# Optimization experiments

Hardware: AMD Instinct MI355X
Metric: run time of the kernel (lower is better)

Reference implementation:

```python
import jax, jax.numpy as jnp
from jax import lax
import numpy as np

HIDDEN = 16
INPUT = 1
OUTPUT = 1
BATCH = 8192
SEQ = 512


def setup_inputs() -> dict:
    key = jax.random.key(0)
    ks = jax.random.split(key, 12)
    s = 1.0 / np.sqrt(HIDDEN)  # PyTorch nn.RNN init scale
    u = lambda k, shape: jax.random.uniform(k, shape, jnp.float32, -s, s)
    return {
        "x": jax.random.normal(ks[0], (BATCH, SEQ, INPUT), jnp.float32),
        "W_ih0": u(ks[1], (HIDDEN, INPUT)),
        "W_hh0": u(ks[2], (HIDDEN, HIDDEN)),
        "b_ih0": u(ks[3], (HIDDEN,)),
        "b_hh0": u(ks[4], (HIDDEN,)),
        "W_ih1": u(ks[5], (HIDDEN, HIDDEN)),
        "W_hh1": u(ks[6], (HIDDEN, HIDDEN)),
        "b_ih1": u(ks[7], (HIDDEN,)),
        "b_hh1": u(ks[8], (HIDDEN,)),
        "W_fc": u(ks[9], (OUTPUT, HIDDEN)),
        "b_fc": u(ks[10], (OUTPUT,)),
    }


def reference(x, W_ih0, W_hh0, b_ih0, b_hh0, W_ih1, W_hh1, b_ih1, b_hh1, W_fc, b_fc):
    # x: [B, S, input]; 2-layer tanh RNN (batch_first), zero initial state,
    # then fc applied to the last timestep of the top layer.
    B = x.shape[0]
    h_init = (jnp.zeros((B, HIDDEN), x.dtype), jnp.zeros((B, HIDDEN), x.dtype))

    def step(carry, xt):  # xt: [B, input]
        h0, h1 = carry
        h0 = jnp.tanh(xt @ W_ih0.T + b_ih0 + h0 @ W_hh0.T + b_hh0)
        h1 = jnp.tanh(h0 @ W_ih1.T + b_ih1 + h1 @ W_hh1.T + b_hh1)
        return (h0, h1), None

    xs = jnp.swapaxes(x, 0, 1)  # [S, B, input] for scan over time
    (h0, h1), _ = lax.scan(step, h_init, xs)
    return h1 @ W_fc.T + b_fc  # [B, output]
```

## Files before the change

### kernel.cpp

```cpp
#include <hip/hip_runtime.h>


#define ROTF(v, K) __int_as_float(__builtin_amdgcn_update_dpp( \
    0, __float_as_int(v), 0x120 + (K), 0xF, 0xF, true))

__device__ __forceinline__ float tanh_fast(float v) {
    float e = __builtin_amdgcn_exp2f(v * 2.8853900817779268f);
    float r = __builtin_amdgcn_rcpf(e + 1.0f);
    return fmaf(-2.0f, r, 1.0f);
}

#define DPPM "row_mask:0xf bank_mask:0xf"

#define MATVEC(acc0, acc1, h, W, init)                                        \
  asm volatile(                                                               \
      "s_nop 1\n\t"                                                           \
      "v_fma_f32 %0, %18, %2, %19\n\t"                                        \
      "v_mul_f32_dpp %1, %18, %3 row_ror:1 " DPPM "\n\t"                      \
      "v_fmac_f32_dpp %0, %18, %4 row_ror:2 " DPPM "\n\t"                     \
      "v_fmac_f32_dpp %1, %18, %5 row_ror:3 " DPPM "\n\t"                     \
      "v_fmac_f32_dpp %0, %18, %6 row_ror:4 " DPPM "\n\t"                     \
      "v_fmac_f32_dpp %1, %18, %7 row_ror:5 " DPPM "\n\t"                     \
      "v_fmac_f32_dpp %0, %18, %8 row_ror:6 " DPPM "\n\t"                     \
      "v_fmac_f32_dpp %1, %18, %9 row_ror:7 " DPPM "\n\t"                     \
      "v_fmac_f32_dpp %0, %18, %10 row_ror:8 " DPPM "\n\t"                    \
      "v_fmac_f32_dpp %1, %18, %11 row_ror:9 " DPPM "\n\t"                    \
      "v_fmac_f32_dpp %0, %18, %12 row_ror:10 " DPPM "\n\t"                   \
      "v_fmac_f32_dpp %1, %18, %13 row_ror:11 " DPPM "\n\t"                   \
      "v_fmac_f32_dpp %0, %18, %14 row_ror:12 " DPPM "\n\t"                   \
      "v_fmac_f32_dpp %1, %18, %15 row_ror:13 " DPPM "\n\t"                   \
      "v_fmac_f32_dpp %0, %18, %16 row_ror:14 " DPPM "\n\t"                   \
      "v_fmac_f32_dpp %1, %18, %17 row_ror:15 " DPPM                         \
      : "=&v"(acc0), "=&v"(acc1)                                              \
      : "v"(W##_0), "v"(W##_1), "v"(W##_2), "v"(W##_3), "v"(W##_4),           \
        "v"(W##_5), "v"(W##_6), "v"(W##_7), "v"(W##_8), "v"(W##_9),           \
        "v"(W##_10), "v"(W##_11), "v"(W##_12), "v"(W##_13), "v"(W##_14),      \
        "v"(W##_15), "v"(h), "v"(init));

#define LOADW(NAME, SRC)                                          \
  const float NAME##_0  = (SRC)[lane * 16 + ((lane -  0) & 15)];  \
  const float NAME##_1  = (SRC)[lane * 16 + ((lane -  1) & 15)];  \
  const float NAME##_2  = (SRC)[lane * 16 + ((lane -  2) & 15)];  \
  const float NAME##_3  = (SRC)[lane * 16 + ((lane -  3) & 15)];  \
  const float NAME##_4  = (SRC)[lane * 16 + ((lane -  4) & 15)];  \
  const float NAME##_5  = (SRC)[lane * 16 + ((lane -  5) & 15)];  \
  const float NAME##_6  = (SRC)[lane * 16 + ((lane -  6) & 15)];  \
  const float NAME##_7  = (SRC)[lane * 16 + ((lane -  7) & 15)];  \
  const float NAME##_8  = (SRC)[lane * 16 + ((lane -  8) & 15)];  \
  const float NAME##_9  = (SRC)[lane * 16 + ((lane -  9) & 15)];  \
  const float NAME##_10 = (SRC)[lane * 16 + ((lane - 10) & 15)];  \
  const float NAME##_11 = (SRC)[lane * 16 + ((lane - 11) & 15)];  \
  const float NAME##_12 = (SRC)[lane * 16 + ((lane - 12) & 15)];  \
  const float NAME##_13 = (SRC)[lane * 16 + ((lane - 13) & 15)];  \
  const float NAME##_14 = (SRC)[lane * 16 + ((lane - 14) & 15)];  \
  const float NAME##_15 = (SRC)[lane * 16 + ((lane - 15) & 15)];

#define STEP(xt)                                         \
  {                                                      \
    const float a_init = fmaf((xt), wih0, bias0);        \
    float a0, a1, c0, c1, d0, d1;                        \
    MATVEC(a0, a1, h0, W0, a_init)                       \
    MATVEC(c0, c1, h1, W2, bias1)                        \
    const float h0n = tanh_fast(a0 + a1);                \
    const float cinit = c0 + c1;                         \
    MATVEC(d0, d1, h0n, W1, cinit)                       \
    h1 = tanh_fast(d0 + d1);                             \
    h0 = h0n;                                            \
  }

__global__ __launch_bounds__(512, 2) void rnn2_kernel(
    const float* __restrict__ x,
    const float* __restrict__ Wih0, const float* __restrict__ Whh0,
    const float* __restrict__ bih0, const float* __restrict__ bhh0,
    const float* __restrict__ Wih1, const float* __restrict__ Whh1,
    const float* __restrict__ bih1, const float* __restrict__ bhh1,
    const float* __restrict__ Wfc,  const float* __restrict__ bfc,
    float* __restrict__ out)
{
    const int tid  = threadIdx.x;
    const int lane = tid & 15;
    const int b    = blockIdx.x * 32 + (tid >> 4);

    LOADW(W0, Whh0)
    LOADW(W1, Wih1)
    LOADW(W2, Whh1)

    const float wih0  = Wih0[lane];
    const float bias0 = bih0[lane] + bhh0[lane];
    const float bias1 = bih1[lane] + bhh1[lane];

    float h0 = 0.0f, h1 = 0.0f;
    const float* xb = x + (size_t)b * 512;

    const float4* xp = reinterpret_cast<const float4*>(xb);
    float4 q0 = xp[0], q1 = xp[1], q2 = xp[2], q3 = xp[3];

    for (int t0 = 0; t0 < 512; t0 += 16) {
        const int tn = (t0 + 16) & 511;
        const float4* xn = reinterpret_cast<const float4*>(xb + tn);
        float4 n0 = xn[0], n1 = xn[1], n2 = xn[2], n3 = xn[3];

        STEP(q0.x) STEP(q0.y) STEP(q0.z) STEP(q0.w)
        STEP(q1.x) STEP(q1.y) STEP(q1.z) STEP(q1.w)
        STEP(q2.x) STEP(q2.y) STEP(q2.z) STEP(q2.w)
        STEP(q3.x) STEP(q3.y) STEP(q3.z) STEP(q3.w)

        q0 = n0; q1 = n1; q2 = n2; q3 = n3;
    }

    float v = h1 * Wfc[lane];
    v += ROTF(v, 8);
    v += ROTF(v, 4);
    v += ROTF(v, 2);
    v += ROTF(v, 1);
    if (lane == 0) out[b] = v + bfc[0];
}

extern "C" void kernel_launch(void* const* d_in, const int* in_sizes, int n_in,
                              void* d_out, int out_size, void* d_ws, size_t ws_size,
                              hipStream_t stream) {
    const float* x    = (const float*)d_in[0];
    const float* Wih0 = (const float*)d_in[1];
    const float* Whh0 = (const float*)d_in[2];
    const float* bih0 = (const float*)d_in[3];
    const float* bhh0 = (const float*)d_in[4];
    const float* Wih1 = (const float*)d_in[5];
    const float* Whh1 = (const float*)d_in[6];
    const float* bih1 = (const float*)d_in[7];
    const float* bhh1 = (const float*)d_in[8];
    const float* Wfc  = (const float*)d_in[9];
    const float* bfc  = (const float*)d_in[10];
    float* out = (float*)d_out;

    rnn2_kernel<<<dim3(256), dim3(512), 0, stream>>>(
        x, Wih0, Whh0, bih0, bhh0, Wih1, Whh1, bih1, bhh1, Wfc, bfc, out);
}
```

Measured before the change: 202.6 us.

## Replace fp32 DPP matvec with packed fp16 dot2 and replicated hidden state

Rewrites each 16x16 recurrent matvec to use packed-fp16 v_dot2_f32_f16 on pre-packed half weight pairs instead of sixteen fp32 DPP fmac instructions. The new hidden state is converted to a half2 pair and replicated into eight rotated registers with DPP moves, so each matvec needs only eight dot2 ops split over two accumulation chains. The intent is to halve the multiply-add instruction count on the serial per-timestep critical path. In exchange it adds DPP replication moves and conversion work, and lowers weight and state precision to fp16, which can accumulate error over 512 timesteps.

```diff
diff --git a/kernel.cpp b/kernel.cpp
--- a/kernel.cpp
+++ b/kernel.cpp
@@ -1,8 +1,24 @@
 #include <hip/hip_runtime.h>
+#include <hip/hip_fp16.h>
 
 
-#define ROTF(v, K) __int_as_float(__builtin_amdgcn_update_dpp( \
-    0, __float_as_int(v), 0x120 + (K), 0xF, 0xF, true))
+typedef _Float16 h2_t __attribute__((ext_vector_type(2)));
+
+#define DPPI(v, CTRL) __builtin_amdgcn_update_dpp(0, (int)(v), (CTRL), 0xF, 0xF, true)
+#define RORL(v, N) ((unsigned int)DPPI((v), 0x120 + (N)))
+#define ROTF(v, K) __int_as_float(DPPI(__float_as_int(v), 0x120 + (K)))
+#define QSWAP_F(v) __int_as_float(DPPI(__float_as_int(v), 0xB1))
+
+__device__ __forceinline__ float fdot2(unsigned int a, unsigned int b, float c) {
+#if __has_builtin(__builtin_amdgcn_fdot2)
+    return __builtin_amdgcn_fdot2(__builtin_bit_cast(h2_t, a),
+                                  __builtin_bit_cast(h2_t, b), c, false);
+#else
+    float r;
+    asm("v_dot2_f32_f16 %0, %1, %2, %3" : "=v"(r) : "v"(a), "v"(b), "v"(c));
+    return r;
+#endif
+}
 
 __device__ __forceinline__ float tanh_fast(float v) {
     float e = __builtin_amdgcn_exp2f(v * 2.8853900817779268f);
@@ -10,62 +26,57 @@
     return fmaf(-2.0f, r, 1.0f);
 }
 
-#define DPPM "row_mask:0xf bank_mask:0xf"
+__device__ __forceinline__ unsigned int pk_w(const float* __restrict__ W,
+                                             int lane, int j) {
+    unsigned int lo = __half_as_ushort(__float2half_rn(W[lane * 16 + j]));
+    unsigned int hi = __half_as_ushort(__float2half_rn(W[lane * 16 + (j ^ 1)]));
+    return (hi << 16) | lo;
+}
 
-#define MATVEC(acc0, acc1, h, W, init)                                        \
-  asm volatile(                                                               \
-      "s_nop 1\n\t"                                                           \
-      "v_fma_f32 %0, %18, %2, %19\n\t"                                        \
-      "v_mul_f32_dpp %1, %18, %3 row_ror:1 " DPPM "\n\t"                      \
-      "v_fmac_f32_dpp %0, %18, %4 row_ror:2 " DPPM "\n\t"                     \
-      "v_fmac_f32_dpp %1, %18, %5 row_ror:3 " DPPM "\n\t"                     \
-      "v_fmac_f32_dpp %0, %18, %6 row_ror:4 " DPPM "\n\t"                     \
-      "v_fmac_f32_dpp %1, %18, %7 row_ror:5 " DPPM "\n\t"                     \
-      "v_fmac_f32_dpp %0, %18, %8 row_ror:6 " DPPM "\n\t"                     \
-      "v_fmac_f32_dpp %1, %18, %9 row_ror:7 " DPPM "\n\t"                     \
-      "v_fmac_f32_dpp %0, %18, %10 row_ror:8 " DPPM "\n\t"                    \
-      "v_fmac_f32_dpp %1, %18, %11 row_ror:9 " DPPM "\n\t"                    \
-      "v_fmac_f32_dpp %0, %18, %12 row_ror:10 " DPPM "\n\t"                   \
-      "v_fmac_f32_dpp %1, %18, %13 row_ror:11 " DPPM "\n\t"                   \
-      "v_fmac_f32_dpp %0, %18, %14 row_ror:12 " DPPM "\n\t"                   \
-      "v_fmac_f32_dpp %1, %18, %15 row_ror:13 " DPPM "\n\t"                   \
-      "v_fmac_f32_dpp %0, %18, %16 row_ror:14 " DPPM "\n\t"                   \
-      "v_fmac_f32_dpp %1, %18, %17 row_ror:15 " DPPM                         \
-      : "=&v"(acc0), "=&v"(acc1)                                              \
-      : "v"(W##_0), "v"(W##_1), "v"(W##_2), "v"(W##_3), "v"(W##_4),           \
-        "v"(W##_5), "v"(W##_6), "v"(W##_7), "v"(W##_8), "v"(W##_9),           \
-        "v"(W##_10), "v"(W##_11), "v"(W##_12), "v"(W##_13), "v"(W##_14),      \
-        "v"(W##_15), "v"(h), "v"(init));
+#define LOADW(NAME, SRC)                                             \
+  const unsigned int NAME##0 = pk_w((SRC), lane, (lane -  0) & 15);  \
+  const unsigned int NAME##1 = pk_w((SRC), lane, (lane -  2) & 15);  \
+  const unsigned int NAME##2 = pk_w((SRC), lane, (lane -  4) & 15);  \
+  const unsigned int NAME##3 = pk_w((SRC), lane, (lane -  6) & 15);  \
+  const unsigned int NAME##4 = pk_w((SRC), lane, (lane -  8) & 15);  \
+  const unsigned int NAME##5 = pk_w((SRC), lane, (lane - 10) & 15);  \
+  const unsigned int NAME##6 = pk_w((SRC), lane, (lane - 12) & 15);  \
+  const unsigned int NAME##7 = pk_w((SRC), lane, (lane - 14) & 15);
 
-#define LOADW(NAME, SRC)                                          \
-  const float NAME##_0  = (SRC)[lane * 16 + ((lane -  0) & 15)];  \
-  const float NAME##_1  = (SRC)[lane * 16 + ((lane -  1) & 15)];  \
-  const float NAME##_2  = (SRC)[lane * 16 + ((lane -  2) & 15)];  \
-  const float NAME##_3  = (SRC)[lane * 16 + ((lane -  3) & 15)];  \
-  const float NAME##_4  = (SRC)[lane * 16 + ((lane -  4) & 15)];  \
-  const float NAME##_5  = (SRC)[lane * 16 + ((lane -  5) & 15)];  \
-  const float NAME##_6  = (SRC)[lane * 16 + ((lane -  6) & 15)];  \
-  const float NAME##_7  = (SRC)[lane * 16 + ((lane -  7) & 15)];  \
-  const float NAME##_8  = (SRC)[lane * 16 + ((lane -  8) & 15)];  \
-  const float NAME##_9  = (SRC)[lane * 16 + ((lane -  9) & 15)];  \
-  const float NAME##_10 = (SRC)[lane * 16 + ((lane - 10) & 15)];  \
-  const float NAME##_11 = (SRC)[lane * 16 + ((lane - 11) & 15)];  \
-  const float NAME##_12 = (SRC)[lane * 16 + ((lane - 12) & 15)];  \
-  const float NAME##_13 = (SRC)[lane * 16 + ((lane - 13) & 15)];  \
-  const float NAME##_14 = (SRC)[lane * 16 + ((lane - 14) & 15)];  \
-  const float NAME##_15 = (SRC)[lane * 16 + ((lane - 15) & 15)];
+#define REPL(hn, R)                                                  \
+  {                                                                  \
+    const float nb_ = QSWAP_F(hn);                                   \
+    R##0 = __builtin_bit_cast(unsigned int,                          \
+             __builtin_amdgcn_cvt_pkrtz((hn), nb_));                 \
+    R##1 = RORL(R##0, 2);   R##2 = RORL(R##0, 4);                    \
+    R##3 = RORL(R##0, 6);   R##4 = RORL(R##0, 8);                    \
+    R##5 = RORL(R##0, 10);  R##6 = RORL(R##0, 12);                   \
+    R##7 = RORL(R##0, 14);                                           \
+  }
 
-#define STEP(xt)                                         \
+#define MV(NAME, R, init, outv)                          \
   {                                                      \
-    const float a_init = fmaf((xt), wih0, bias0);        \
-    float a0, a1, c0, c1, d0, d1;                        \
-    MATVEC(a0, a1, h0, W0, a_init)                       \
-    MATVEC(c0, c1, h1, W2, bias1)                        \
-    const float h0n = tanh_fast(a0 + a1);                \
-    const float cinit = c0 + c1;                         \
-    MATVEC(d0, d1, h0n, W1, cinit)                       \
-    h1 = tanh_fast(d0 + d1);                             \
-    h0 = h0n;                                            \
+    float m0_ = fdot2(NAME##0, R##0, (init));            \
+    float m1_ = fdot2(NAME##1, R##1, 0.0f);              \
+    m0_ = fdot2(NAME##2, R##2, m0_);                     \
+    m1_ = fdot2(NAME##3, R##3, m1_);                     \
+    m0_ = fdot2(NAME##4, R##4, m0_);                     \
+    m1_ = fdot2(NAME##5, R##5, m1_);                     \
+    m0_ = fdot2(NAME##6, R##6, m0_);                     \
+    m1_ = fdot2(NAME##7, R##7, m1_);                     \
+    outv = m0_ + m1_;                                    \
+  }
+
+#define STEP(xt)                                   \
+  {                                                \
+    float a_, c_, d_;                              \
+    MV(W0, A, fmaf((xt), wih0, bias0), a_)         \
+    MV(W2, B, bias1, c_)                           \
+    const float h0n_ = tanh_fast(a_);              \
+    REPL(h0n_, A)                                  \
+    MV(W1, A, c_, d_)                              \
+    h1s = tanh_fast(d_);                           \
+    REPL(h1s, B)                                   \
   }
 
 __global__ __launch_bounds__(512, 2) void rnn2_kernel(
@@ -89,9 +100,11 @@
     const float bias0 = bih0[lane] + bhh0[lane];
     const float bias1 = bih1[lane] + bhh1[lane];
 
-    float h0 = 0.0f, h1 = 0.0f;
+    unsigned int A0 = 0, A1 = 0, A2 = 0, A3 = 0, A4 = 0, A5 = 0, A6 = 0, A7 = 0;
+    unsigned int B0 = 0, B1 = 0, B2 = 0, B3 = 0, B4 = 0, B5 = 0, B6 = 0, B7 = 0;
+    float h1s = 0.0f;
+
     const float* xb = x + (size_t)b * 512;
-
     const float4* xp = reinterpret_cast<const float4*>(xb);
     float4 q0 = xp[0], q1 = xp[1], q2 = xp[2], q3 = xp[3];
 
@@ -108,7 +121,7 @@
         q0 = n0; q1 = n1; q2 = n2; q3 = n3;
     }
 
-    float v = h1 * Wfc[lane];
+    float v = h1s * Wfc[lane];
     v += ROTF(v, 8);
     v += ROTF(v, 4);
     v += ROTF(v, 2);
```

Measured after the change: 201.0 us. About the same (-0.8%).
